# Performance work log

Measured on AMD Instinct MI355X. Metric: run time of the kernel, lower is better.

Reference implementation:

```python
import jax, jax.numpy as jnp
import numpy as np

EMBED = 256
HEADS = 8
LEVELS = 4
POINTS = 4
HD = EMBED // HEADS  # 32
SHAPES = np.array([[100, 100], [50, 50], [25, 25], [13, 13]], dtype=np.int64)  # (H_l, W_l)


def setup_inputs() -> dict:
    key = jax.random.key(0)
    ks = jax.random.split(key, 12)
    nv = int(SHAPES.prod(-1).sum())  # 13294
    bs, nq, d = 2, nv, EMBED
    level_start = np.concatenate([[0], SHAPES.prod(-1).cumsum()[:-1]])
    s = 0.02
    return {
        "query": jax.random.normal(ks[0], (bs, nq, d), jnp.float32),
        "reference_points": jax.random.uniform(ks[1], (bs, nq, LEVELS, 2), jnp.float32),
        "value": jax.random.normal(ks[2], (bs, nv, d), jnp.float32),
        "spatial_shapes": jnp.asarray(SHAPES, jnp.int32),
        "level_start_index": jnp.asarray(level_start, jnp.int32),
        "key_padding_mask": jnp.zeros((bs, nv), jnp.bool_),
        "W_samp": jax.random.normal(ks[3], (HEADS * LEVELS * POINTS * 2, d), jnp.float32) * s,
        "b_samp": jax.random.normal(ks[4], (HEADS * LEVELS * POINTS * 2,), jnp.float32),
        "W_attn": jax.random.normal(ks[5], (HEADS * LEVELS * POINTS, d), jnp.float32) * s,
        "b_attn": jnp.zeros((HEADS * LEVELS * POINTS,), jnp.float32),
        "W_val": jax.random.normal(ks[6], (d, d), jnp.float32) * s,
        "b_val": jnp.zeros((d,), jnp.float32),
        "W_out": jax.random.normal(ks[7], (d, d), jnp.float32) * s,
        "b_out": jnp.zeros((d,), jnp.float32),
    }


def _msda_core(value_bhnd, shapes_np, starts_np, loc, attn):
    """value_bhnd: (bs, H, nv, hd); loc: (bs, nq, H, L, P, 2) in [0,1]; attn: (bs, nq, H, L, P)."""
    bs, heads, nv, hd = value_bhnd.shape
    nq = loc.shape[1]
    out = jnp.zeros((bs, nq, heads, hd), value_bhnd.dtype)
    for l in range(LEVELS):
        H, W = int(shapes_np[l, 0]), int(shapes_np[l, 1])
        start = int(starts_np[l])
        v = jax.lax.dynamic_slice_in_dim(value_bhnd, start, H * W, axis=2)  # (bs, heads, H*W, hd)
        # grid_sample(align_corners=False): pixel coord = loc * size - 0.5
        lx = loc[:, :, :, l, :, 0] * W - 0.5  # (bs, nq, heads, P)
        ly = loc[:, :, :, l, :, 1] * H - 0.5
        x0 = jnp.floor(lx)
        y0 = jnp.floor(ly)
        tx = lx - x0
        ty = ly - y0
        x0i = x0.astype(jnp.int32)
        y0i = y0.astype(jnp.int32)
        samp = jnp.zeros((bs, heads, nq, POINTS, hd), value_bhnd.dtype)
        for dy, wy in ((0, 1.0 - ty), (1, ty)):
            for dx, wx in ((0, 1.0 - tx), (1, tx)):
                xi = x0i + dx
                yi = y0i + dy
                valid = (xi >= 0) & (xi < W) & (yi >= 0) & (yi < H)  # zeros padding
                idx = jnp.clip(yi, 0, H - 1) * W + jnp.clip(xi, 0, W - 1)  # (bs, nq, heads, P)
                idx_t = idx.transpose(0, 2, 1, 3).reshape(bs, heads, nq * POINTS)
                g = jnp.take_along_axis(v, idx_t[..., None], axis=2)
                g = g.reshape(bs, heads, nq, POINTS, hd)
                w = jnp.where(valid, wx * wy, 0.0).transpose(0, 2, 1, 3)[..., None]
                samp = samp + g * w
        out = out + jnp.einsum("bhqpd,bqhp->bqhd", samp, attn[:, :, :, l, :])
    return out.reshape(bs, nq, heads * hd)


def reference(query, reference_points, value, spatial_shapes, level_start_index,
              key_padding_mask, W_samp, b_samp, W_attn, b_attn, W_val, b_val, W_out, b_out):
    bs, nq, d = query.shape
    v = value @ W_val.T + b_val
    v = jnp.where(key_padding_mask[..., None], 0.0, v)
    v = v.reshape(bs, -1, HEADS, HD).transpose(0, 2, 1, 3)  # (bs, heads, nv, hd)
    off = (query @ W_samp.T + b_samp).reshape(bs, nq, HEADS, LEVELS, POINTS, 2)
    attn = (query @ W_attn.T + b_attn).reshape(bs, nq, HEADS, LEVELS * POINTS)
    attn = jax.nn.softmax(attn, axis=-1).reshape(bs, nq, HEADS, LEVELS, POINTS)
    ss = np.asarray(spatial_shapes)
    starts = np.asarray(level_start_index)
    # offset normalizer is (W, H) per level
    norm = jnp.asarray(ss[:, ::-1].copy(), jnp.float32)
    loc = reference_points[:, :, None, :, None, :] + off / norm[None, None, None, :, None, :]
    out = _msda_core(v, ss, starts, loc, attn)
    return out @ W_out.T + b_out
```

## Files before the change

kernel.cpp:

```cpp
#include <hip/hip_runtime.h>
#include <hip/hip_fp16.h>
#include <cstdint>
#include <cstddef>

#define EMBED  256
#define NV_PER_B 13294
#define M_PAD   26624
#define NQPB   8

__constant__ const int c_H[4]  = {100, 50, 25, 13};
__constant__ const int c_W[4]  = {100, 50, 25, 13};
__constant__ const int c_ST[4] = {0, 10000, 12500, 13125};

typedef _Float16 f16x8 __attribute__((ext_vector_type(8)));
typedef float f32x4 __attribute__((ext_vector_type(4)));

#define GLDS(g, l) __builtin_amdgcn_global_load_lds( \
    (const __attribute__((address_space(1))) void*)(g), \
    (__attribute__((address_space(3))) void*)(l), 16, 0, 0)

__device__ inline unsigned short f2hu(float x) { return __half_as_ushort(__float2half(x)); }

__global__ __launch_bounds__(256) void convert_kernel(
    const float* __restrict__ q,  const float* __restrict__ v,
    const float* __restrict__ wv, const float* __restrict__ wsamp,
    const float* __restrict__ wattn, const float* __restrict__ wo,
    const float* __restrict__ bsamp, const float* __restrict__ battn,
    __half* __restrict__ q_h, __half* __restrict__ v_h,
    __half* __restrict__ wv_h, __half* __restrict__ wcat_h,
    __half* __restrict__ wo_h, float* __restrict__ bias_cat,
    int n_real4, int n_pad4)
{
    const int i = blockIdx.x * 256 + threadIdx.x;
    if (i < n_pad4) {
        float4 a = make_float4(0.f, 0.f, 0.f, 0.f);
        float4 b = make_float4(0.f, 0.f, 0.f, 0.f);
        if (i < n_real4) {
            a = ((const float4*)q)[i];
            b = ((const float4*)v)[i];
        }
        ((ushort4*)q_h)[i] = make_ushort4(f2hu(a.x), f2hu(a.y), f2hu(a.z), f2hu(a.w));
        ((ushort4*)v_h)[i] = make_ushort4(f2hu(b.x), f2hu(b.y), f2hu(b.z), f2hu(b.w));
    }
    if (i < 16384) {
        float4 a = ((const float4*)wv)[i];
        float4 c = ((const float4*)wo)[i];
        ((ushort4*)wv_h)[i] = make_ushort4(f2hu(a.x), f2hu(a.y), f2hu(a.z), f2hu(a.w));
        ((ushort4*)wo_h)[i] = make_ushort4(f2hu(c.x), f2hu(c.y), f2hu(c.z), f2hu(c.w));
    }
    if (i < 24576) {
        float4 a = (i < 16384) ? ((const float4*)wsamp)[i]
                               : ((const float4*)wattn)[i - 16384];
        ((ushort4*)wcat_h)[i] = make_ushort4(f2hu(a.x), f2hu(a.y), f2hu(a.z), f2hu(a.w));
    }
    if (i < 96) {
        float4 a = (i < 64) ? ((const float4*)bsamp)[i]
                            : ((const float4*)battn)[i - 64];
        ((float4*)bias_cat)[i] = a;
    }
}

__device__ __forceinline__ void wave_kloop(
    const __half* __restrict__ A, const __half* __restrict__ Wt,
    size_t aoff, size_t boff, char* myst, f32x4 (&acc)[4][4],
    int lr16, int qk)
{
    auto issue = [&](int stage, int kc) {
        char* sa = myst + stage * 8192;
        const __half* ap = A + aoff + kc * 32;
        const __half* bp = Wt + boff + kc * 32;
        #pragma unroll
        for (int g = 0; g < 4; ++g) GLDS(ap + g * (16 * 256), sa + g * 1024);
        #pragma unroll
        for (int g = 0; g < 4; ++g) GLDS(bp + g * (16 * 256), sa + 4096 + g * 1024);
    };

    issue(0, 0);
    issue(1, 1);
    #pragma unroll
    for (int it = 0; it < 8; ++it) {
        if (it < 7) asm volatile("s_waitcnt vmcnt(8)" ::: "memory");
        else        asm volatile("s_waitcnt vmcnt(0)" ::: "memory");
        const char* sa = myst + (it & 1) * 8192;
        f16x8 af[4], bfr[4];
        #pragma unroll
        for (int mi = 0; mi < 4; ++mi)
            af[mi] = *(const f16x8*)(sa + (mi * 16 + lr16) * 64 + qk * 16);
        #pragma unroll
        for (int ni = 0; ni < 4; ++ni)
            bfr[ni] = *(const f16x8*)(sa + 4096 + (ni * 16 + lr16) * 64 + qk * 16);
        asm volatile("s_waitcnt lgkmcnt(0)" ::: "memory");
        if (it + 2 < 8) issue(it & 1, it + 2);
        #pragma unroll
        for (int mi = 0; mi < 4; ++mi)
            #pragma unroll
            for (int ni = 0; ni < 4; ++ni)
                acc[mi][ni] = __builtin_amdgcn_mfma_f32_16x16x32_f16(
                    af[mi], bfr[ni], acc[mi][ni], 0, 0, 0);
    }
}

__global__ __launch_bounds__(256) void proj_gemm_kernel(
    const __half* __restrict__ v_h, const __half* __restrict__ wv_h,
    const float* __restrict__ b_val, __half* __restrict__ vproj,
    const __half* __restrict__ q_h, const __half* __restrict__ wcat_h,
    const float* __restrict__ bias_cat, __half* __restrict__ qo)
{
    __shared__ __align__(16) char smem[65536];
    const int t = threadIdx.x;
    const int wave = t >> 6, lane = t & 63;
    const int lr16 = lane & 15, qk = lane >> 4;
    const int wrow = wave & 1, wcol = wave >> 1;
    const int y = blockIdx.y;
    const int bm = blockIdx.x * 128;

    const __half* A; const __half* Wt; const float* bias; __half* Cc; int Nst, bn;
    if (y < 2) { A = v_h; Wt = wv_h;   bias = b_val;    Cc = vproj; Nst = 256; bn = y * 128; }
    else       { A = q_h; Wt = wcat_h; bias = bias_cat; Cc = qo;    Nst = 384; bn = (y - 2) * 128; }

    char* myst = smem + wave * 16384;
    const int srow = lane >> 2, skb = lane & 3;
    const size_t aoff = (size_t)(bm + wrow * 64 + srow) * 256 + skb * 8;
    const size_t boff = (size_t)(bn + wcol * 64 + srow) * 256 + skb * 8;

    f32x4 acc[4][4] = {};
    wave_kloop(A, Wt, aoff, boff, myst, acc, lr16, qk);

    const int colbase = bn + wcol * 64;
    float bv[4];
    #pragma unroll
    for (int ni = 0; ni < 4; ++ni) bv[ni] = bias[colbase + ni * 16 + lr16];
    __half* ep = (__half*)myst;
    #pragma unroll
    for (int mi = 0; mi < 4; ++mi)
        #pragma unroll
        for (int ni = 0; ni < 4; ++ni)
            #pragma unroll
            for (int r = 0; r < 4; ++r)
                ep[(mi * 16 + qk * 4 + r) * 72 + ni * 16 + lr16] =
                    __float2half(acc[mi][ni][r] + bv[ni]);
    const int er = lane >> 3, ec = (lane & 7) * 8;
    #pragma unroll
    for (int pass = 0; pass < 8; ++pass) {
        const int r = pass * 8 + er;
        const int4 vv = *(const int4*)&ep[r * 72 + ec];
        const int grow = bm + wrow * 64 + r;
        *(int4*)&Cc[(size_t)grow * Nst + colbase + ec] = vv;
    }
}

__global__ __launch_bounds__(256) void gemm_out_kernel(
    const __half* __restrict__ core, const __half* __restrict__ wo_h,
    const float* __restrict__ b_out, float* __restrict__ C, int M)
{
    __shared__ __align__(16) char smem[65536];
    const int t = threadIdx.x;
    const int wave = t >> 6, lane = t & 63;
    const int lr16 = lane & 15, qk = lane >> 4;
    const int wrow = wave & 1, wcol = wave >> 1;
    const int bm = blockIdx.x * 128, bn = blockIdx.y * 128;

    char* myst = smem + wave * 16384;
    const int srow = lane >> 2, skb = lane & 3;
    const size_t aoff = (size_t)(bm + wrow * 64 + srow) * 256 + skb * 8;
    const size_t boff = (size_t)(bn + wcol * 64 + srow) * 256 + skb * 8;

    f32x4 acc[4][4] = {};
    wave_kloop(core, wo_h, aoff, boff, myst, acc, lr16, qk);

    const int colbase = bn + wcol * 64;
    float bv[4];
    #pragma unroll
    for (int ni = 0; ni < 4; ++ni) bv[ni] = b_out[colbase + ni * 16 + lr16];
    float* ep = (float*)myst;
    const int er = lane >> 4, ec = (lane & 15) * 4;
    #pragma unroll
    for (int p = 0; p < 4; ++p) {
        #pragma unroll
        for (int ni = 0; ni < 4; ++ni)
            #pragma unroll
            for (int r = 0; r < 4; ++r)
                ep[(qk * 4 + r) * 68 + ni * 16 + lr16] = acc[p][ni][r] + bv[ni];
        #pragma unroll
        for (int j = 0; j < 4; ++j) {
            const int r16 = j * 4 + er;
            const float4 vv = *(const float4*)&ep[r16 * 68 + ec];
            const int grow = bm + wrow * 64 + p * 16 + r16;
            if (grow < M)
                *(float4*)&C[(size_t)grow * 256 + colbase + ec] = vv;
        }
        asm volatile("s_waitcnt lgkmcnt(0)" ::: "memory");
    }
}

__global__ __launch_bounds__(256, 4) void msda_core_kernel(
    const __half* __restrict__ vproj,
    const float* __restrict__ refp,
    const __half* __restrict__ qo,
    __half* __restrict__ core,
    int nq, int nv, int M)
{
    const int bq0 = blockIdx.x * NQPB;
    const int t = threadIdx.x;

    __shared__ float s_w[NQPB * 128];
    __shared__ float s_ref[NQPB * 8];
    __shared__ __align__(16) unsigned int s_tap[NQPB * 8][68];

    #pragma unroll
    for (int i = 0; i < 4; ++i) {
        const int s = t + i * 256;
        const int q = s >> 7, r = s & 127;
        s_w[s] = __half2float(qo[(size_t)(bq0 + q) * 384 + 256 + r]);
    }
    if (t < NQPB * 8) {
        const int gq = min(bq0 + (t >> 3), M - 1);
        s_ref[t] = refp[(size_t)gq * 8 + (t & 7)];
    }
    __syncthreads();

    if (t < NQPB * 8) {
        const int base = (t >> 3) * 128 + (t & 7) * 16;
        float m = -1e30f;
        #pragma unroll
        for (int j = 0; j < 16; ++j) m = fmaxf(m, s_w[base + j]);
        float e[16]; float ssum = 0.f;
        #pragma unroll
        for (int j = 0; j < 16; ++j) { e[j] = expf(s_w[base + j] - m); ssum += e[j]; }
        const float inv = 1.f / ssum;
        #pragma unroll
        for (int j = 0; j < 16; ++j) s_w[base + j] = e[j] * inv;
    }
    __syncthreads();

    #pragma unroll
    for (int i = 0; i < 4; ++i) {
        const int s = t + i * 256;
        const int q = s >> 7, r = s & 127;
        const int h = r >> 4, lp = r & 15, l = lp >> 2;
        const int gq = bq0 + q;
        const float2 off = __half22float2(*(const __half2*)&qo[(size_t)gq * 384 + r * 2]);
        const float rx = s_ref[q * 8 + l * 2];
        const float ry = s_ref[q * 8 + l * 2 + 1];
        const int W = c_W[l], H = c_H[l], st = c_ST[l];
        const float fW = (float)W, fH = (float)H;
        const float lx = (rx + off.x / fW) * fW - 0.5f;
        const float ly = (ry + off.y / fH) * fH - 0.5f;
        const float x0f = floorf(lx), y0f = floorf(ly);
        const float fx = lx - x0f, fy = ly - y0f;
        const int x0 = (int)x0f, y0 = (int)y0f;
        const float aw = s_w[s];
        const float wx[2] = {1.f - fx, fx};
        const float wy[2] = {1.f - fy, fy};
        #pragma unroll
        for (int dy = 0; dy < 2; ++dy) {
            #pragma unroll
            for (int dx = 0; dx < 2; ++dx) {
                const int xi = x0 + dx, yi = y0 + dy;
                const bool ok = (xi >= 0) & (xi < W) & (yi >= 0) & (yi < H);
                const unsigned int idx = ok ? (unsigned int)(st + yi * W + xi) : 0u;
                const float w = ok ? aw * wy[dy] * wx[dx] : 0.f;
                const unsigned int pw = (unsigned int)f2hu(w);
                s_tap[q * 8 + h][lp * 4 + dy * 2 + dx] = idx | (pw << 16);
            }
        }
    }
    __syncthreads();

    const int q   = t >> 5;
    const int l32 = t & 31;
    const int h   = l32 >> 2;
    const int c8  = l32 & 3;
    const int gq  = bq0 + q;
    const int b   = (gq >= nq) ? 1 : 0;
    const __half* __restrict__ vb = vproj + (size_t)b * nv * EMBED + h * 32 + c8 * 8;
    const uint4* __restrict__ tapq = (const uint4*)s_tap[q * 8 + h];

    __align__(16) __half2 acc2[4];
    #pragma unroll
    for (int i = 0; i < 4; ++i) acc2[i] = __float2half2_rn(0.f);

    #pragma unroll 2
    for (int g = 0; g < 16; ++g) {
        const uint4 tq = tapq[g];
        const int4 r0 = *(const int4*)(vb + (size_t)(tq.x & 0xFFFFu) * EMBED);
        const int4 r1 = *(const int4*)(vb + (size_t)(tq.y & 0xFFFFu) * EMBED);
        const int4 r2 = *(const int4*)(vb + (size_t)(tq.z & 0xFFFFu) * EMBED);
        const int4 r3 = *(const int4*)(vb + (size_t)(tq.w & 0xFFFFu) * EMBED);
        const __half2 w0 = __half2half2(__ushort_as_half((unsigned short)(tq.x >> 16)));
        const __half2 w1 = __half2half2(__ushort_as_half((unsigned short)(tq.y >> 16)));
        const __half2 w2 = __half2half2(__ushort_as_half((unsigned short)(tq.z >> 16)));
        const __half2 w3 = __half2half2(__ushort_as_half((unsigned short)(tq.w >> 16)));
        const __half2* h0 = (const __half2*)&r0;
        const __half2* h1 = (const __half2*)&r1;
        const __half2* h2 = (const __half2*)&r2;
        const __half2* h3 = (const __half2*)&r3;
        #pragma unroll
        for (int i = 0; i < 4; ++i) {
            acc2[i] = __hfma2(w0, h0[i], acc2[i]);
            acc2[i] = __hfma2(w1, h1[i], acc2[i]);
            acc2[i] = __hfma2(w2, h2[i], acc2[i]);
            acc2[i] = __hfma2(w3, h3[i], acc2[i]);
        }
    }

    if (gq < M)
        *(int4*)&core[(size_t)gq * 256 + h * 32 + c8 * 8] = *(const int4*)acc2;
}

extern "C" void kernel_launch(void* const* d_in, const int* in_sizes, int n_in,
                              void* d_out, int out_size, void* d_ws, size_t ws_size,
                              hipStream_t stream) {
    const float* query  = (const float*)d_in[0];
    const float* refp   = (const float*)d_in[1];
    const float* value  = (const float*)d_in[2];
    const float* W_samp = (const float*)d_in[6];
    const float* b_samp = (const float*)d_in[7];
    const float* W_attn = (const float*)d_in[8];
    const float* b_attn = (const float*)d_in[9];
    const float* W_val  = (const float*)d_in[10];
    const float* b_val  = (const float*)d_in[11];
    const float* W_out  = (const float*)d_in[12];
    const float* b_out  = (const float*)d_in[13];
    float* out = (float*)d_out;

    const int M  = in_sizes[0] / EMBED;
    const int nq = NV_PER_B;
    const int nv = NV_PER_B;
    const int Mp = M_PAD;

    char* p = (char*)d_ws;
    __half* coreh  = (__half*)p; p += (size_t)Mp * 256 * 2;
    __half* vproj  = (__half*)p; p += (size_t)Mp * 256 * 2;
    __half* qo     = (__half*)p; p += (size_t)Mp * 384 * 2;
    __half* q_h    = (__half*)p; p += (size_t)Mp * 256 * 2;
    __half* v_h    = (__half*)p; p += (size_t)Mp * 256 * 2;
    __half* wv_h   = (__half*)p; p += 65536 * 2;
    __half* wcat_h = (__half*)p; p += 98304 * 2;
    __half* wo_h   = (__half*)p; p += 65536 * 2;
    float*  biascat= (float*)p;  p += 384 * 4;

    const int n_real4 = M * 256 / 4;
    const int n_pad4  = Mp * 256 / 4;
    dim3 blk(256);

    convert_kernel<<<dim3((n_pad4 + 255) / 256), blk, 0, stream>>>(
        query, value, W_val, W_samp, W_attn, W_out, b_samp, b_attn,
        q_h, v_h, wv_h, wcat_h, wo_h, biascat, n_real4, n_pad4);

    const int mb = Mp / 128;
    proj_gemm_kernel<<<dim3(mb, 5), blk, 0, stream>>>(
        v_h, wv_h, b_val, vproj, q_h, wcat_h, biascat, qo);

    msda_core_kernel<<<dim3((M + NQPB - 1) / NQPB), blk, 0, stream>>>(
        vproj, refp, qo, coreh, nq, nv, M);

    gemm_out_kernel<<<dim3(mb, 2), blk, 0, stream>>>(
        coreh, wo_h, b_out, out, M);
}
```

Measured before the change: 206.7 us.

## Fuse output projection into sampling kernel and pre-tile GEMM operands

Removes the separate output GEMM kernel. Each sampling block now keeps its 8-query core result in shared memory and multiplies it by W_out with MFMA, writing the final fp32 output directly, which avoids the round-trip of the core tensor through global memory. The convert kernel also now writes q, v and the weights in a tiled, k-chunked layout through a shared-memory transpose, so the projection GEMM's global-to-LDS loads are contiguous 512-element chunks. The trade-off is that the fused GEMM tile is poorly shaped: only 8 of 16 MFMA columns are used, and W_out fragments are read from global or L2 by every block.

```diff
diff --git a/kernel.cpp b/kernel.cpp
--- a/kernel.cpp
+++ b/kernel.cpp
@@ -19,114 +19,129 @@
     (const __attribute__((address_space(1))) void*)(g), \
     (__attribute__((address_space(3))) void*)(l), 16, 0, 0)
 
-__device__ inline unsigned short f2hu(float x) { return __half_as_ushort(__float2half(x)); }
 
 __global__ __launch_bounds__(256) void convert_kernel(
     const float* __restrict__ q,  const float* __restrict__ v,
     const float* __restrict__ wv, const float* __restrict__ wsamp,
     const float* __restrict__ wattn, const float* __restrict__ wo,
     const float* __restrict__ bsamp, const float* __restrict__ battn,
-    __half* __restrict__ q_h, __half* __restrict__ v_h,
-    __half* __restrict__ wv_h, __half* __restrict__ wcat_h,
-    __half* __restrict__ wo_h, float* __restrict__ bias_cat,
-    int n_real4, int n_pad4)
+    __half* __restrict__ q_t, __half* __restrict__ v_t,
+    __half* __restrict__ wv_t, __half* __restrict__ wcat_t,
+    __half* __restrict__ wo_h, float* __restrict__ biascat, int M)
 {
-    const int i = blockIdx.x * 256 + threadIdx.x;
-    if (i < n_pad4) {
+    __shared__ float ls[64][36];
+    const int id = blockIdx.x, t = threadIdx.x;
+
+    if (id < 6736) {
+        const float* srcA; const float* srcB = nullptr;
+        __half* dst; int tile, kc, vrows, part2 = 0;
+        if (id < 6656) {
+            const int arr = id & 1, r = id >> 1;
+            tile = r >> 3; kc = r & 7;
+            srcA = arr ? v : q; dst = arr ? v_t : q_t; vrows = M;
+        } else if (id < 6688) {
+            const int r = id - 6656;
+            tile = r >> 3; kc = r & 7;
+            srcA = wv; dst = wv_t; vrows = 256;
+        } else {
+            const int r = id - 6688;
+            tile = r >> 3; kc = r & 7;
+            srcA = wsamp; srcB = wattn; dst = wcat_t; vrows = 384; part2 = 1;
+        }
+        const int row = t >> 2, kq = t & 3;
+        const int gr = tile * 64 + row;
         float4 a = make_float4(0.f, 0.f, 0.f, 0.f);
         float4 b = make_float4(0.f, 0.f, 0.f, 0.f);
-        if (i < n_real4) {
-            a = ((const float4*)q)[i];
-            b = ((const float4*)v)[i];
-        }
-        ((ushort4*)q_h)[i] = make_ushort4(f2hu(a.x), f2hu(a.y), f2hu(a.z), f2hu(a.w));
-        ((ushort4*)v_h)[i] = make_ushort4(f2hu(b.x), f2hu(b.y), f2hu(b.z), f2hu(b.w));
-    }
-    if (i < 16384) {
-        float4 a = ((const float4*)wv)[i];
-        float4 c = ((const float4*)wo)[i];
-        ((ushort4*)wv_h)[i] = make_ushort4(f2hu(a.x), f2hu(a.y), f2hu(a.z), f2hu(a.w));
-        ((ushort4*)wo_h)[i] = make_ushort4(f2hu(c.x), f2hu(c.y), f2hu(c.z), f2hu(c.w));
-    }
-    if (i < 24576) {
-        float4 a = (i < 16384) ? ((const float4*)wsamp)[i]
-                               : ((const float4*)wattn)[i - 16384];
-        ((ushort4*)wcat_h)[i] = make_ushort4(f2hu(a.x), f2hu(a.y), f2hu(a.z), f2hu(a.w));
-    }
-    if (i < 96) {
-        float4 a = (i < 64) ? ((const float4*)bsamp)[i]
-                            : ((const float4*)battn)[i - 64];
-        ((float4*)bias_cat)[i] = a;
+        if (gr < vrows) {
+            const float* sp = (part2 && gr >= 256) ? (srcB + (size_t)(gr - 256) * 256)
+                                                   : (srcA + (size_t)gr * 256);
+            a = *(const float4*)(sp + kc * 32 + kq * 8);
+            b = *(const float4*)(sp + kc * 32 + kq * 8 + 4);
+        }
+        *(float4*)&ls[row][kq * 8]     = a;
+        *(float4*)&ls[row][kq * 8 + 4] = b;
+        __syncthreads();
+        const int g = t >> 6, r2 = t & 63;
+        __align__(16) __half h8[8];
+        #pragma unroll
+        for (int j = 0; j < 8; ++j) h8[j] = __float2half(ls[r2][g * 8 + j]);
+        *(int4*)(dst + (size_t)tile * 16384 + kc * 2048 + g * 512 + r2 * 8) = *(const int4*)h8;
+    } else if (id < 6768) {
+        const int i = (id - 6736) * 256 + t;
+        const float4 a = ((const float4*)wo)[i * 2];
+        const float4 b = ((const float4*)wo)[i * 2 + 1];
+        __align__(16) __half h8[8];
+        h8[0] = __float2half(a.x); h8[1] = __float2half(a.y);
+        h8[2] = __float2half(a.z); h8[3] = __float2half(a.w);
+        h8[4] = __float2half(b.x); h8[5] = __float2half(b.y);
+        h8[6] = __float2half(b.z); h8[7] = __float2half(b.w);
+        *(int4*)(wo_h + (size_t)i * 8) = *(const int4*)h8;
+    } else {
+        if (t < 96) {
+            const float4 a = (t < 64) ? ((const float4*)bsamp)[t]
+                                      : ((const float4*)battn)[t - 64];
+            ((float4*)biascat)[t] = a;
+        }
     }
 }
 
-__device__ __forceinline__ void wave_kloop(
-    const __half* __restrict__ A, const __half* __restrict__ Wt,
-    size_t aoff, size_t boff, char* myst, f32x4 (&acc)[4][4],
-    int lr16, int qk)
-{
-    auto issue = [&](int stage, int kc) {
-        char* sa = myst + stage * 8192;
-        const __half* ap = A + aoff + kc * 32;
-        const __half* bp = Wt + boff + kc * 32;
-        #pragma unroll
-        for (int g = 0; g < 4; ++g) GLDS(ap + g * (16 * 256), sa + g * 1024);
-        #pragma unroll
-        for (int g = 0; g < 4; ++g) GLDS(bp + g * (16 * 256), sa + 4096 + g * 1024);
-    };
-
-    issue(0, 0);
-    issue(1, 1);
-    #pragma unroll
-    for (int it = 0; it < 8; ++it) {
-        if (it < 7) asm volatile("s_waitcnt vmcnt(8)" ::: "memory");
-        else        asm volatile("s_waitcnt vmcnt(0)" ::: "memory");
-        const char* sa = myst + (it & 1) * 8192;
-        f16x8 af[4], bfr[4];
-        #pragma unroll
-        for (int mi = 0; mi < 4; ++mi)
-            af[mi] = *(const f16x8*)(sa + (mi * 16 + lr16) * 64 + qk * 16);
-        #pragma unroll
-        for (int ni = 0; ni < 4; ++ni)
-            bfr[ni] = *(const f16x8*)(sa + 4096 + (ni * 16 + lr16) * 64 + qk * 16);
-        asm volatile("s_waitcnt lgkmcnt(0)" ::: "memory");
-        if (it + 2 < 8) issue(it & 1, it + 2);
-        #pragma unroll
-        for (int mi = 0; mi < 4; ++mi)
-            #pragma unroll
-            for (int ni = 0; ni < 4; ++ni)
-                acc[mi][ni] = __builtin_amdgcn_mfma_f32_16x16x32_f16(
-                    af[mi], bfr[ni], acc[mi][ni], 0, 0, 0);
-    }
-}
-
 __global__ __launch_bounds__(256) void proj_gemm_kernel(
-    const __half* __restrict__ v_h, const __half* __restrict__ wv_h,
-    const float* __restrict__ b_val, __half* __restrict__ vproj,
-    const __half* __restrict__ q_h, const __half* __restrict__ wcat_h,
-    const float* __restrict__ bias_cat, __half* __restrict__ qo)
+    const __half* __restrict__ q_t, const __half* __restrict__ v_t,
+    const __half* __restrict__ wv_t, const __half* __restrict__ wcat_t,
+    const float* __restrict__ b_val, const float* __restrict__ biascat,
+    __half* __restrict__ vproj, __half* __restrict__ qo)
 {
     __shared__ __align__(16) char smem[65536];
     const int t = threadIdx.x;
     const int wave = t >> 6, lane = t & 63;
     const int lr16 = lane & 15, qk = lane >> 4;
     const int wrow = wave & 1, wcol = wave >> 1;
-    const int y = blockIdx.y;
-    const int bm = blockIdx.x * 128;
-
-    const __half* A; const __half* Wt; const float* bias; __half* Cc; int Nst, bn;
-    if (y < 2) { A = v_h; Wt = wv_h;   bias = b_val;    Cc = vproj; Nst = 256; bn = y * 128; }
-    else       { A = q_h; Wt = wcat_h; bias = bias_cat; Cc = qo;    Nst = 384; bn = (y - 2) * 128; }
+    const int y = blockIdx.y, bx = blockIdx.x;
+
+    const __half* At; const __half* Bt; const float* bias; __half* Cc; int Nst, tb;
+    if (y < 2) { At = v_t; Bt = wv_t;   bias = b_val;   Cc = vproj; Nst = 256; tb = y * 2 + wcol; }
+    else       { At = q_t; Bt = wcat_t; bias = biascat; Cc = qo;    Nst = 384; tb = (y - 2) * 2 + wcol; }
+    const int ta = bx * 2 + wrow;
 
     char* myst = smem + wave * 16384;
-    const int srow = lane >> 2, skb = lane & 3;
-    const size_t aoff = (size_t)(bm + wrow * 64 + srow) * 256 + skb * 8;
-    const size_t boff = (size_t)(bn + wcol * 64 + srow) * 256 + skb * 8;
+    const __half* abase = At + (size_t)ta * 16384 + lane * 8;
+    const __half* bbase = Bt + (size_t)tb * 16384 + lane * 8;
+
+    auto issue = [&](int stage, int kc) {
+        char* sa = myst + stage * 8192;
+        #pragma unroll
+        for (int g = 0; g < 4; ++g) GLDS(abase + kc * 2048 + g * 512, sa + g * 1024);
+        #pragma unroll
+        for (int g = 0; g < 4; ++g) GLDS(bbase + kc * 2048 + g * 512, sa + 4096 + g * 1024);
+    };
 
     f32x4 acc[4][4] = {};
-    wave_kloop(A, Wt, aoff, boff, myst, acc, lr16, qk);
-
-    const int colbase = bn + wcol * 64;
+    issue(0, 0);
+    issue(1, 1);
+    #pragma unroll
+    for (int it = 0; it < 8; ++it) {
+        if (it < 7) asm volatile("s_waitcnt vmcnt(8)" ::: "memory");
+        else        asm volatile("s_waitcnt vmcnt(0)" ::: "memory");
+        const char* sa = myst + (it & 1) * 8192;
+        const char* sb = sa + 4096;
+        f16x8 af[4], bfr[4];
+        #pragma unroll
+        for (int mi = 0; mi < 4; ++mi)
+            af[mi] = *(const f16x8*)(sa + qk * 1024 + (mi * 16 + lr16) * 16);
+        #pragma unroll
+        for (int ni = 0; ni < 4; ++ni)
+            bfr[ni] = *(const f16x8*)(sb + qk * 1024 + (ni * 16 + lr16) * 16);
+        asm volatile("s_waitcnt lgkmcnt(0)" ::: "memory");
+        if (it + 2 < 8) issue(it & 1, it + 2);
+        #pragma unroll
+        for (int mi = 0; mi < 4; ++mi)
+            #pragma unroll
+            for (int ni = 0; ni < 4; ++ni)
+                acc[mi][ni] = __builtin_amdgcn_mfma_f32_16x16x32_f16(
+                    af[mi], bfr[ni], acc[mi][ni], 0, 0, 0);
+    }
+
+    const int colbase = tb * 64;
     float bv[4];
     #pragma unroll
     for (int ni = 0; ni < 4; ++ni) bv[ni] = bias[colbase + ni * 16 + lr16];
@@ -144,52 +159,8 @@
     for (int pass = 0; pass < 8; ++pass) {
         const int r = pass * 8 + er;
         const int4 vv = *(const int4*)&ep[r * 72 + ec];
-        const int grow = bm + wrow * 64 + r;
+        const int grow = bx * 128 + wrow * 64 + r;
         *(int4*)&Cc[(size_t)grow * Nst + colbase + ec] = vv;
-    }
-}
-
-__global__ __launch_bounds__(256) void gemm_out_kernel(
-    const __half* __restrict__ core, const __half* __restrict__ wo_h,
-    const float* __restrict__ b_out, float* __restrict__ C, int M)
-{
-    __shared__ __align__(16) char smem[65536];
-    const int t = threadIdx.x;
-    const int wave = t >> 6, lane = t & 63;
-    const int lr16 = lane & 15, qk = lane >> 4;
-    const int wrow = wave & 1, wcol = wave >> 1;
-    const int bm = blockIdx.x * 128, bn = blockIdx.y * 128;
-
-    char* myst = smem + wave * 16384;
-    const int srow = lane >> 2, skb = lane & 3;
-    const size_t aoff = (size_t)(bm + wrow * 64 + srow) * 256 + skb * 8;
-    const size_t boff = (size_t)(bn + wcol * 64 + srow) * 256 + skb * 8;
-
-    f32x4 acc[4][4] = {};
-    wave_kloop(core, wo_h, aoff, boff, myst, acc, lr16, qk);
-
-    const int colbase = bn + wcol * 64;
-    float bv[4];
-    #pragma unroll
-    for (int ni = 0; ni < 4; ++ni) bv[ni] = b_out[colbase + ni * 16 + lr16];
-    float* ep = (float*)myst;
-    const int er = lane >> 4, ec = (lane & 15) * 4;
-    #pragma unroll
-    for (int p = 0; p < 4; ++p) {
-        #pragma unroll
-        for (int ni = 0; ni < 4; ++ni)
-            #pragma unroll
-            for (int r = 0; r < 4; ++r)
-                ep[(qk * 4 + r) * 68 + ni * 16 + lr16] = acc[p][ni][r] + bv[ni];
-        #pragma unroll
-        for (int j = 0; j < 4; ++j) {
-            const int r16 = j * 4 + er;
-            const float4 vv = *(const float4*)&ep[r16 * 68 + ec];
-            const int grow = bm + wrow * 64 + p * 16 + r16;
-            if (grow < M)
-                *(float4*)&C[(size_t)grow * 256 + colbase + ec] = vv;
-        }
-        asm volatile("s_waitcnt lgkmcnt(0)" ::: "memory");
     }
 }
 
@@ -197,7 +168,9 @@
     const __half* __restrict__ vproj,
     const float* __restrict__ refp,
     const __half* __restrict__ qo,
-    __half* __restrict__ core,
+    const __half* __restrict__ wo_h,
+    const float* __restrict__ b_out,
+    float* __restrict__ out,
     int nq, int nv, int M)
 {
     const int bq0 = blockIdx.x * NQPB;
@@ -206,6 +179,7 @@
     __shared__ float s_w[NQPB * 128];
     __shared__ float s_ref[NQPB * 8];
     __shared__ __align__(16) unsigned int s_tap[NQPB * 8][68];
+    __shared__ __align__(16) __half s_core[16 * 272];
 
     #pragma unroll
     for (int i = 0; i < 4; ++i) {
@@ -260,52 +234,84 @@
                 const bool ok = (xi >= 0) & (xi < W) & (yi >= 0) & (yi < H);
                 const unsigned int idx = ok ? (unsigned int)(st + yi * W + xi) : 0u;
                 const float w = ok ? aw * wy[dy] * wx[dx] : 0.f;
-                const unsigned int pw = (unsigned int)f2hu(w);
+                const unsigned int pw = (unsigned int)__half_as_ushort(__float2half(w));
                 s_tap[q * 8 + h][lp * 4 + dy * 2 + dx] = idx | (pw << 16);
             }
         }
     }
     __syncthreads();
 
-    const int q   = t >> 5;
-    const int l32 = t & 31;
-    const int h   = l32 >> 2;
-    const int c8  = l32 & 3;
-    const int gq  = bq0 + q;
-    const int b   = (gq >= nq) ? 1 : 0;
-    const __half* __restrict__ vb = vproj + (size_t)b * nv * EMBED + h * 32 + c8 * 8;
-    const uint4* __restrict__ tapq = (const uint4*)s_tap[q * 8 + h];
-
-    __align__(16) __half2 acc2[4];
-    #pragma unroll
-    for (int i = 0; i < 4; ++i) acc2[i] = __float2half2_rn(0.f);
-
-    #pragma unroll 2
-    for (int g = 0; g < 16; ++g) {
-        const uint4 tq = tapq[g];
-        const int4 r0 = *(const int4*)(vb + (size_t)(tq.x & 0xFFFFu) * EMBED);
-        const int4 r1 = *(const int4*)(vb + (size_t)(tq.y & 0xFFFFu) * EMBED);
-        const int4 r2 = *(const int4*)(vb + (size_t)(tq.z & 0xFFFFu) * EMBED);
-        const int4 r3 = *(const int4*)(vb + (size_t)(tq.w & 0xFFFFu) * EMBED);
-        const __half2 w0 = __half2half2(__ushort_as_half((unsigned short)(tq.x >> 16)));
-        const __half2 w1 = __half2half2(__ushort_as_half((unsigned short)(tq.y >> 16)));
-        const __half2 w2 = __half2half2(__ushort_as_half((unsigned short)(tq.z >> 16)));
-        const __half2 w3 = __half2half2(__ushort_as_half((unsigned short)(tq.w >> 16)));
-        const __half2* h0 = (const __half2*)&r0;
-        const __half2* h1 = (const __half2*)&r1;
-        const __half2* h2 = (const __half2*)&r2;
-        const __half2* h3 = (const __half2*)&r3;
-        #pragma unroll
-        for (int i = 0; i < 4; ++i) {
-            acc2[i] = __hfma2(w0, h0[i], acc2[i]);
-            acc2[i] = __hfma2(w1, h1[i], acc2[i]);
-            acc2[i] = __hfma2(w2, h2[i], acc2[i]);
-            acc2[i] = __hfma2(w3, h3[i], acc2[i]);
-        }
-    }
-
-    if (gq < M)
-        *(int4*)&core[(size_t)gq * 256 + h * 32 + c8 * 8] = *(const int4*)acc2;
+    {
+        const int q   = t >> 5;
+        const int l32 = t & 31;
+        const int h   = l32 >> 2;
+        const int c8  = l32 & 3;
+        const int gq  = bq0 + q;
+        const int b   = (gq >= nq) ? 1 : 0;
+        const __half* __restrict__ vb = vproj + (size_t)b * nv * EMBED + h * 32 + c8 * 8;
+        const uint4* __restrict__ tapq = (const uint4*)s_tap[q * 8 + h];
+
+        __align__(16) __half2 acc2[4];
+        #pragma unroll
+        for (int i = 0; i < 4; ++i) acc2[i] = __float2half2_rn(0.f);
+
+        #pragma unroll 2
+        for (int g = 0; g < 16; ++g) {
+            const uint4 tq = tapq[g];
+            const int4 r0 = *(const int4*)(vb + (size_t)(tq.x & 0xFFFFu) * EMBED);
+            const int4 r1 = *(const int4*)(vb + (size_t)(tq.y & 0xFFFFu) * EMBED);
+            const int4 r2 = *(const int4*)(vb + (size_t)(tq.z & 0xFFFFu) * EMBED);
+            const int4 r3 = *(const int4*)(vb + (size_t)(tq.w & 0xFFFFu) * EMBED);
+            const __half2 w0 = __half2half2(__ushort_as_half((unsigned short)(tq.x >> 16)));
+            const __half2 w1 = __half2half2(__ushort_as_half((unsigned short)(tq.y >> 16)));
+            const __half2 w2 = __half2half2(__ushort_as_half((unsigned short)(tq.z >> 16)));
+            const __half2 w3 = __half2half2(__ushort_as_half((unsigned short)(tq.w >> 16)));
+            const __half2* h0 = (const __half2*)&r0;
+            const __half2* h1 = (const __half2*)&r1;
+            const __half2* h2 = (const __half2*)&r2;
+            const __half2* h3 = (const __half2*)&r3;
+            #pragma unroll
+            for (int i = 0; i < 4; ++i) {
+                acc2[i] = __hfma2(w0, h0[i], acc2[i]);
+                acc2[i] = __hfma2(w1, h1[i], acc2[i]);
+                acc2[i] = __hfma2(w2, h2[i], acc2[i]);
+                acc2[i] = __hfma2(w3, h3[i], acc2[i]);
+            }
+        }
+        *(int4*)(s_core + q * 272 + h * 32 + c8 * 8) = *(const int4*)acc2;
+    }
+    __syncthreads();
+
+    {
+        const int w = t >> 6;
+        const int lane = t & 63;
+        const int lr16 = lane & 15, qk = lane >> 4;
+        const char* cb = (const char*)s_core;
+        f32x4 oacc[4] = {};
+        #pragma unroll 2
+        for (int kit = 0; kit < 8; ++kit) {
+            const f16x8 bfrag = *(const f16x8*)(cb + lr16 * 544 + kit * 64 + qk * 16);
+            #pragma unroll
+            for (int mi = 0; mi < 4; ++mi) {
+                const f16x8 afrag = *(const f16x8*)(wo_h +
+                    (size_t)(w * 64 + mi * 16 + lr16) * 256 + kit * 32 + qk * 8);
+                oacc[mi] = __builtin_amdgcn_mfma_f32_16x16x32_f16(
+                    afrag, bfrag, oacc[mi], 0, 0, 0);
+            }
+        }
+        const int gq2 = bq0 + lr16;
+        if (lr16 < NQPB && gq2 < M) {
+            #pragma unroll
+            for (int mi = 0; mi < 4; ++mi) {
+                const int col = w * 64 + mi * 16 + qk * 4;
+                const float4 b4 = *(const float4*)&b_out[col];
+                float4 o;
+                o.x = oacc[mi][0] + b4.x; o.y = oacc[mi][1] + b4.y;
+                o.z = oacc[mi][2] + b4.z; o.w = oacc[mi][3] + b4.w;
+                *(float4*)&out[(size_t)gq2 * 256 + col] = o;
+            }
+        }
+    }
 }
 
 extern "C" void kernel_launch(void* const* d_in, const int* in_sizes, int n_in,
@@ -330,31 +336,24 @@
     const int Mp = M_PAD;
 
     char* p = (char*)d_ws;
-    __half* coreh  = (__half*)p; p += (size_t)Mp * 256 * 2;
+    __half* q_t    = (__half*)p; p += (size_t)Mp * 256 * 2;
+    __half* v_t    = (__half*)p; p += (size_t)Mp * 256 * 2;
     __half* vproj  = (__half*)p; p += (size_t)Mp * 256 * 2;
     __half* qo     = (__half*)p; p += (size_t)Mp * 384 * 2;
-    __half* q_h    = (__half*)p; p += (size_t)Mp * 256 * 2;
-    __half* v_h    = (__half*)p; p += (size_t)Mp * 256 * 2;
-    __half* wv_h   = (__half*)p; p += 65536 * 2;
-    __half* wcat_h = (__half*)p; p += 98304 * 2;
+    __half* wv_t   = (__half*)p; p += 65536 * 2;
+    __half* wcat_t = (__half*)p; p += 98304 * 2;
     __half* wo_h   = (__half*)p; p += 65536 * 2;
     float*  biascat= (float*)p;  p += 384 * 4;
 
-    const int n_real4 = M * 256 / 4;
-    const int n_pad4  = Mp * 256 / 4;
     dim3 blk(256);
 
-    convert_kernel<<<dim3((n_pad4 + 255) / 256), blk, 0, stream>>>(
+    convert_kernel<<<dim3(6769), blk, 0, stream>>>(
         query, value, W_val, W_samp, W_attn, W_out, b_samp, b_attn,
-        q_h, v_h, wv_h, wcat_h, wo_h, biascat, n_real4, n_pad4);
-
-    const int mb = Mp / 128;
-    proj_gemm_kernel<<<dim3(mb, 5), blk, 0, stream>>>(
-        v_h, wv_h, b_val, vproj, q_h, wcat_h, biascat, qo);
+        q_t, v_t, wv_t, wcat_t, wo_h, biascat, M);
+
+    proj_gemm_kernel<<<dim3(Mp / 128, 5), blk, 0, stream>>>(
+        q_t, v_t, wv_t, wcat_t, b_val, biascat, vproj, qo);
 
     msda_core_kernel<<<dim3((M + NQPB - 1) / NQPB), blk, 0, stream>>>(
-        vproj, refp, qo, coreh, nq, nv, M);
-
-    gemm_out_kernel<<<dim3(mb, 2), blk, 0, stream>>>(
-        coreh, wo_h, b_out, out, M);
+        vproj, refp, qo, wo_h, b_out, out, nq, nv, M);
 }
```

New measurement: 237.2 us. 1.15x slower.
